# Performance work log

Measured on AMD Instinct MI355X. Metric: run time of the kernel, lower is better.

## Reference

```python
import jax, jax.numpy as jnp
import numpy as np

D_MODEL = 1024
NUM_HEADS = 16
D_K = D_MODEL // NUM_HEADS
ROPE_THETA = 10000.0


def apply_rope(x, pos):
    # x: [B, nh, S, d_k], pos: [S]
    d = x.shape[-1]
    inv_freq = ROPE_THETA ** (-jnp.arange(0, d, 2, dtype=jnp.float32) / d)  # [d/2]
    ang = pos.astype(jnp.float32)[:, None] * inv_freq[None, :]              # [S, d/2]
    cos, sin = jnp.cos(ang), jnp.sin(ang)
    x1, x2 = x[..., 0::2], x[..., 1::2]
    out_even = x1 * cos - x2 * sin
    out_odd = x1 * sin + x2 * cos
    return jnp.stack([out_even, out_odd], axis=-1).reshape(x.shape)


def setup_inputs() -> dict:
    key = jax.random.key(0)
    kx, kq, kk, kv, ko = jax.random.split(key, 5)
    B, S = 4, 2048
    std = np.sqrt(2.0 / (D_MODEL + D_MODEL))
    x = jax.random.normal(kx, (B, S, D_MODEL), dtype=jnp.float32)
    q_proj = jax.random.normal(kq, (D_MODEL, D_MODEL), dtype=jnp.float32) * std
    k_proj = jax.random.normal(kk, (D_MODEL, D_MODEL), dtype=jnp.float32) * std
    v_proj = jax.random.normal(kv, (D_MODEL, D_MODEL), dtype=jnp.float32) * std
    o_proj = jax.random.normal(ko, (D_MODEL, D_MODEL), dtype=jnp.float32) * std
    return {"x": x, "q_proj": q_proj, "k_proj": k_proj, "v_proj": v_proj, "o_proj": o_proj}


def reference(x, q_proj, k_proj, v_proj, o_proj):
    B, S, D = x.shape
    nh, dk = NUM_HEADS, D // NUM_HEADS
    # projections: weights stored [d_out, d_in] -> x @ W.T
    def split_heads(t):
        return t.reshape(B, S, nh, dk).transpose(0, 2, 1, 3)  # [B, nh, S, dk]
    q = split_heads(x @ q_proj.T)
    k = split_heads(x @ k_proj.T)
    v = split_heads(x @ v_proj.T)
    pos = jnp.arange(S)
    q = apply_rope(q, pos)
    k = apply_rope(k, pos)
    scores = jnp.einsum('bhqd,bhkd->bhqk', q, k) / jnp.sqrt(jnp.float32(dk))
    causal = jnp.tril(jnp.ones((S, S), dtype=bool))
    scores = jnp.where(causal, scores, -jnp.inf)
    attn = jax.nn.softmax(scores, axis=-1)
    out = jnp.einsum('bhqk,bhkd->bhqd', attn, v)          # [B, nh, S, dk]
    out = out.transpose(0, 2, 1, 3).reshape(B, S, D)      # merge heads
    return out @ o_proj.T
```

## Files before the change

### kernel.cpp

```cpp
#include <hip/hip_runtime.h>
#include <hip/hip_bf16.h>
#include <cstdint>


typedef __attribute__((ext_vector_type(8))) short short8;
typedef __attribute__((ext_vector_type(4))) float float4v;

#define MFMA16(a, b, c) __builtin_amdgcn_mfma_f32_16x16x32_bf16((a), (b), (c), 0, 0, 0)

__device__ __forceinline__ void glds16(const void* g, void* l) {
    __builtin_amdgcn_global_load_lds(
        (const __attribute__((address_space(1))) void*)g,
        (__attribute__((address_space(3))) void*)l, 16, 0, 0);
}

__device__ __forceinline__ unsigned int pk2(float a, float b) {
    __hip_bfloat162 h = __float22bfloat162_rn(make_float2(a, b));
    union { __hip_bfloat162 h; unsigned int u; } v; v.h = h;
    return v.u;
}

__device__ __forceinline__ unsigned short f2bf(float x) {
    union { float f; unsigned int u; } v; v.f = x;
    unsigned int r = (v.u + 0x7FFFu + ((v.u >> 16) & 1u)) >> 16;
    return (unsigned short)r;
}

__device__ __forceinline__ float bf2f(unsigned short b) {
    union { unsigned int u; float f; } v; v.u = ((unsigned int)b) << 16;
    return v.f;
}

__device__ __forceinline__ short8 load8f(const float* p) {
    const float4 f0 = *(const float4*)p;
    const float4 f1 = *(const float4*)(p + 4);
    union { short8 s; unsigned int u[4]; } r;
    r.u[0] = pk2(f0.x, f0.y);
    r.u[1] = pk2(f0.z, f0.w);
    r.u[2] = pk2(f1.x, f1.y);
    r.u[3] = pk2(f1.z, f1.w);
    return r.s;
}

__global__ __launch_bounds__(256) void convert_kernel(
    const float* __restrict__ in, __hip_bfloat16* __restrict__ out)
{
    const int idx = (blockIdx.x * 256 + threadIdx.x) * 8;
    *(short8*)(out + idx) = load8f(in + idx);
}

__global__ __launch_bounds__(256) void convert4_kernel(
    const float* __restrict__ a, const float* __restrict__ b,
    const float* __restrict__ c, const float* __restrict__ d,
    __hip_bfloat16* __restrict__ oa, __hip_bfloat16* __restrict__ ob,
    __hip_bfloat16* __restrict__ oc, __hip_bfloat16* __restrict__ od)
{
    const int m = blockIdx.x >> 9;
    const float* in = (m == 0) ? a : (m == 1) ? b : (m == 2) ? c : d;
    __hip_bfloat16* out = (m == 0) ? oa : (m == 1) ? ob : (m == 2) ? oc : od;
    const int idx = ((blockIdx.x & 511) * 256 + threadIdx.x) * 8;
    *(short8*)(out + idx) = load8f(in + idx);
}

__global__ __launch_bounds__(256) void rope_table_kernel(float2* __restrict__ table)
{
    const int idx = blockIdx.x * 256 + threadIdx.x;
    const int pos = idx >> 5, fi = idx & 31;
    const float f = exp2f(-(float)fi * (13.287712379549449f / 32.0f));
    float sn, cs;
    sincosf((float)pos * f, &sn, &cs);
    table[idx] = make_float2(cs, sn);
}

__global__ __launch_bounds__(256) void rope2_kernel(
    __hip_bfloat16* __restrict__ Qp, __hip_bfloat16* __restrict__ Kp,
    const float2* __restrict__ table)
{
    const int sel = blockIdx.x >> 14;
    __hip_bfloat16* T = sel ? Kp : Qp;
    const float scale = sel ? 1.0f : 0.18033688011112042f;
    const int idx = (blockIdx.x & 16383) * 256 + threadIdx.x;
    const int r = idx >> 9;
    const int p = idx & 511;
    const int h = p >> 5, i = p & 31;
    const float2 cs = table[(r & 2047) * 32 + i];
    unsigned short* ptr = (unsigned short*)T + (int64_t)r * 1024 + h * 64 + 2 * i;
    const ushort2 xv = *(const ushort2*)ptr;
    const float x1 = bf2f(xv.x), x2 = bf2f(xv.y);
    const unsigned int o = pk2((x1 * cs.x - x2 * cs.y) * scale,
                               (x1 * cs.y + x2 * cs.x) * scale);
    *(unsigned int*)ptr = o;
}

template<int BBF>
__global__ __launch_bounds__(256) void qkv_gemm(
    const __hip_bfloat16* __restrict__ Abf,
    const void* __restrict__ Wq, const void* __restrict__ Wk, const void* __restrict__ Wv,
    __hip_bfloat16* __restrict__ Qp, __hip_bfloat16* __restrict__ Kp,
    __hip_bfloat16* __restrict__ Vt)
{
    __shared__ unsigned short smem[128 * 128];

    const int K = 1024;
    const int bm = blockIdx.x / 24, bn = blockIdx.x % 24;
    const int widx = bn >> 3;
    const int bcol0 = (bn & 7) * 128;
    const void* W = (widx == 0) ? Wq : (widx == 1) ? Wk : Wv;

    const int tid = threadIdx.x;
    const int wave = tid >> 6, lane = tid & 63;
    const int wm = (wave >> 1) * 64, wn = (wave & 1) * 64;
    const int m16 = lane & 15, quad = lane >> 4;

    const int lrow = lane >> 2, lcol = (lane & 3) * 8;
    const int srow = tid >> 2, scol = (tid & 3) * 8;

    float4v acc[4][4] = {};

    for (int k0 = 0; k0 < K; k0 += 32) {
        short8 rb0, rb1;
        if (!BBF) {
            const float* Wf = (const float*)W;
            rb0 = load8f(Wf + (int64_t)(bcol0 + srow) * K + scol + k0);
            rb1 = load8f(Wf + (int64_t)(bcol0 + 64 + srow) * K + scol + k0);
        }
        __syncthreads();
        {
            const __hip_bfloat16* g = Abf + (int64_t)(bm * 128 + wave * 32 + lrow) * K + lcol + k0;
            glds16(g, &smem[wave * 1024]);
            glds16(g + (int64_t)16 * K, &smem[wave * 1024 + 512]);
        }
        if (BBF) {
            const __hip_bfloat16* g = (const __hip_bfloat16*)W +
                (int64_t)(bcol0 + wave * 32 + lrow) * K + lcol + k0;
            glds16(g, &smem[4096 + wave * 1024]);
            glds16(g + (int64_t)16 * K, &smem[4096 + wave * 1024 + 512]);
        } else {
            *(short8*)&smem[4096 + srow * 32 + scol] = rb0;
            *(short8*)&smem[4096 + (64 + srow) * 32 + scol] = rb1;
        }
        __syncthreads();

        short8 af[4], bf[4];
#pragma unroll
        for (int i = 0; i < 4; i++)
            af[i] = *(const short8*)&smem[(wm + i * 16 + m16) * 32 + quad * 8];
#pragma unroll
        for (int j = 0; j < 4; j++)
            bf[j] = *(const short8*)&smem[4096 + (wn + j * 16 + m16) * 32 + quad * 8];
#pragma unroll
        for (int i = 0; i < 4; i++)
#pragma unroll
            for (int j = 0; j < 4; j++)
                acc[i][j] = MFMA16(af[i], bf[j], acc[i][j]);
    }

    if (widx == 2) {
        __syncthreads();
#pragma unroll
        for (int i = 0; i < 4; i++)
#pragma unroll
            for (int j = 0; j < 4; j++) {
                const int col = wn + j * 16 + m16;
                const int key = (col & 7) * 8;
#pragma unroll
                for (int r = 0; r < 4; r++) {
                    const int row = wm + i * 16 + quad * 4 + r;
                    smem[col * 128 + (row ^ key)] = f2bf(acc[i][j][r]);
                }
            }
        __syncthreads();
        const int dc = tid >> 4;
        const int seg = (tid & 15) * 8;
#pragma unroll
        for (int pass = 0; pass < 8; pass++) {
            const int dcol = pass * 16 + dc;
            const short8 v = *(const short8*)&smem[dcol * 128 + (seg ^ ((dcol & 7) * 8))];
            *(short8*)((unsigned short*)Vt + (int64_t)(bcol0 + dcol) * 8192 + bm * 128 + seg) = v;
        }
    } else {
        __hip_bfloat16* dst = (widx == 0) ? Qp : Kp;
        const int row0 = bm * 128 + wm + quad * 4;
        const int col0 = bcol0 + wn + m16;
#pragma unroll
        for (int i = 0; i < 4; i++)
#pragma unroll
            for (int j = 0; j < 4; j++)
#pragma unroll
                for (int r = 0; r < 4; r++)
                    dst[(int64_t)(row0 + i * 16 + r) * 1024 + col0 + j * 16] =
                        __float2bfloat16(acc[i][j][r]);
    }
}

template<int BBF>
__global__ __launch_bounds__(256) void gemm_o(
    const __hip_bfloat16* __restrict__ Abf, const void* __restrict__ B,
    float* __restrict__ C, int M, int N, int K)
{
    __shared__ __hip_bfloat16 lA[128 * 32];
    __shared__ __hip_bfloat16 lB[64 * 32];

    const int nb = N >> 6;
    const int bm = blockIdx.x / nb, bn = blockIdx.x % nb;
    const int tid = threadIdx.x;
    const int wave = tid >> 6, lane = tid & 63;
    const int wm = (wave >> 1) * 64, wn = (wave & 1) * 32;
    const int m16 = lane & 15, quad = lane >> 4;
    const int lrow = lane >> 2, lcol = (lane & 3) * 8;
    const int srow = tid >> 2, scol = (tid & 3) * 8;

    float4v acc[4][2] = {};

    for (int k0 = 0; k0 < K; k0 += 32) {
        short8 rb0;
        if (!BBF) {
            const float* Bf = (const float*)B;
            rb0 = load8f(Bf + (int64_t)(bn * 64 + srow) * K + scol + k0);
        }
        __syncthreads();
        {
            const __hip_bfloat16* g = Abf + (int64_t)(bm * 128 + wave * 32 + lrow) * K + lcol + k0;
            glds16(g, &lA[wave * 1024]);
            glds16(g + (int64_t)16 * K, &lA[wave * 1024 + 512]);
        }
        if (BBF) {
            glds16((const __hip_bfloat16*)B +
                   (int64_t)(bn * 64 + wave * 16 + (lane >> 2)) * K + lcol + k0,
                   &lB[wave * 512]);
        } else {
            *(short8*)&lB[srow * 32 + scol] = rb0;
        }
        __syncthreads();

        short8 af[4], bf[2];
#pragma unroll
        for (int i = 0; i < 4; i++)
            af[i] = *(const short8*)&lA[(wm + i * 16 + m16) * 32 + quad * 8];
#pragma unroll
        for (int j = 0; j < 2; j++)
            bf[j] = *(const short8*)&lB[(wn + j * 16 + m16) * 32 + quad * 8];
#pragma unroll
        for (int i = 0; i < 4; i++)
#pragma unroll
            for (int j = 0; j < 2; j++)
                acc[i][j] = MFMA16(af[i], bf[j], acc[i][j]);
    }

    const int row0 = bm * 128 + wm + quad * 4;
    const int col0 = bn * 64 + wn + m16;
#pragma unroll
    for (int i = 0; i < 4; i++)
#pragma unroll
        for (int j = 0; j < 2; j++)
#pragma unroll
            for (int r = 0; r < 4; r++)
                C[(int64_t)(row0 + i * 16 + r) * N + col0 + j * 16] = acc[i][j][r];
}

__global__ __launch_bounds__(256) void attn_kernel(
    const __hip_bfloat16* __restrict__ Q,
    const __hip_bfloat16* __restrict__ Kg,
    const __hip_bfloat16* __restrict__ Vt,
    __hip_bfloat16* __restrict__ O,
    int S, int BS)
{
    const int g = blockIdx.x >> 6;
    const int qt = (g < 4) ? 15 - g : (g < 8) ? 11 - g : (g < 12) ? g : g - 12;
    const int bh = blockIdx.x & 63;
    const int b = bh >> 4, h = bh & 15;
    const int tid = threadIdx.x;
    const int wave = tid >> 6, lane = tid & 63;
    const int m16 = lane & 15, quad = lane >> 4;

    __shared__ __hip_bfloat16 lK[64 * 64];
    __shared__ __hip_bfloat16 lV[64 * 64];
    __shared__ __hip_bfloat16 lP[4][32 * 64];

    const int qrow0 = qt * 128 + wave * 32;
    const int64_t rowbase = (int64_t)b * S;

    short8 aq[2][2];
#pragma unroll
    for (int i = 0; i < 2; i++) {
        const __hip_bfloat16* qp = Q + (rowbase + qrow0 + i * 16 + m16) * 1024 + h * 64 + quad * 8;
        aq[i][0] = *(const short8*)qp;
        aq[i][1] = *(const short8*)(qp + 32);
    }

    float lsum[2] = {0.f, 0.f};
    float4v o_acc[2][4] = {};

    const int srow = tid >> 3;
    const int scol = (tid & 7) * 8;

    const int ktmax_blk = 2 * qt + 1;
    const int ktmax_w = 2 * qt + (wave >> 1);
    const int k8 = (m16 & 7) * 8;

    short8 pk0, pk1, pv0, pv1;
#define PREFETCH(KT)                                                                          \
    do {                                                                                      \
        pk0 = *(const short8*)(Kg + (rowbase + (KT) * 64 + srow) * 1024 + h * 64 + scol);     \
        pk1 = *(const short8*)(Kg + (rowbase + (KT) * 64 + srow + 32) * 1024 + h * 64 + scol);\
        pv0 = *(const short8*)(Vt + (int64_t)(h * 64 + srow) * BS + rowbase + (KT) * 64 + scol);      \
        pv1 = *(const short8*)(Vt + (int64_t)(h * 64 + srow + 32) * BS + rowbase + (KT) * 64 + scol); \
    } while (0)

    PREFETCH(0);

    for (int kt = 0; kt <= ktmax_blk; kt++) {
        __syncthreads();
        *(short8*)&lK[srow * 64 + (scol ^ ((srow & 7) * 8))] = pk0;
        *(short8*)&lK[(srow + 32) * 64 + (scol ^ (((srow + 32) & 7) * 8))] = pk1;
        *(short8*)&lV[srow * 64 + (scol ^ ((srow & 7) * 8))] = pv0;
        *(short8*)&lV[(srow + 32) * 64 + (scol ^ (((srow + 32) & 7) * 8))] = pv1;
        __syncthreads();

        if (kt < ktmax_blk) PREFETCH(kt + 1);

        if (kt <= ktmax_w) {
            float4v st[4][2] = {};
#pragma unroll
            for (int mi = 0; mi < 4; mi++) {
                const int n = mi * 16 + m16;
                const int sw = (n & 7) * 8;
                short8 k0 = *(const short8*)&lK[n * 64 + ((quad * 8) ^ sw)];
                short8 k1 = *(const short8*)&lK[n * 64 + ((32 + quad * 8) ^ sw)];
#pragma unroll
                for (int ni = 0; ni < 2; ni++) {
                    st[mi][ni] = MFMA16(k0, aq[ni][0], st[mi][ni]);
                    st[mi][ni] = MFMA16(k1, aq[ni][1], st[mi][ni]);
                }
            }

            const bool need_mask = (kt * 64 + 63 > qrow0);
#pragma unroll
            for (int ni = 0; ni < 2; ni++) {
                const int qg = qrow0 + ni * 16 + m16;
#pragma unroll
                for (int mi = 0; mi < 4; mi++) {
                    float p[4];
#pragma unroll
                    for (int r = 0; r < 4; r++) {
                        p[r] = exp2f(st[mi][ni][r]);
                        if (need_mask) {
                            const int kvg = kt * 64 + mi * 16 + quad * 4 + r;
                            if (kvg > qg) p[r] = 0.0f;
                        }
                    }
                    lsum[ni] += (p[0] + p[1]) + (p[2] + p[3]);
                    uint2 w;
                    w.x = pk2(p[0], p[1]);
                    w.y = pk2(p[2], p[3]);
                    *(uint2*)&lP[wave][(ni * 16 + m16) * 64 + ((mi * 16 + quad * 4) ^ k8)] = w;
                }
            }

            short8 ap[2][2];
#pragma unroll
            for (int i = 0; i < 2; i++)
#pragma unroll
                for (int ks = 0; ks < 2; ks++)
                    ap[i][ks] = *(const short8*)
                        &lP[wave][(i * 16 + m16) * 64 + ((ks * 32 + quad * 8) ^ k8)];
#pragma unroll
            for (int jd = 0; jd < 4; jd++) {
                const int d = jd * 16 + m16;
                const int sw = (d & 7) * 8;
                short8 b0 = *(const short8*)&lV[d * 64 + ((quad * 8) ^ sw)];
                short8 b1 = *(const short8*)&lV[d * 64 + ((32 + quad * 8) ^ sw)];
#pragma unroll
                for (int i = 0; i < 2; i++) {
                    o_acc[i][jd] = MFMA16(ap[i][0], b0, o_acc[i][jd]);
                    o_acc[i][jd] = MFMA16(ap[i][1], b1, o_acc[i][jd]);
                }
            }
        }
    }
#undef PREFETCH

    float rinv[2];
#pragma unroll
    for (int ni = 0; ni < 2; ni++) {
        float v = lsum[ni];
        v += __shfl_xor(v, 16);
        v += __shfl_xor(v, 32);
        rinv[ni] = 1.0f / v;
    }
    float ri[2][4];
#pragma unroll
    for (int i = 0; i < 2; i++)
#pragma unroll
        for (int r = 0; r < 4; r++)
            ri[i][r] = __shfl(rinv[i], quad * 4 + r);

#pragma unroll
    for (int i = 0; i < 2; i++)
#pragma unroll
        for (int jd = 0; jd < 4; jd++)
#pragma unroll
            for (int r = 0; r < 4; r++) {
                const int row = qrow0 + i * 16 + quad * 4 + r;
                O[(rowbase + row) * 1024 + h * 64 + jd * 16 + m16] =
                    __float2bfloat16(o_acc[i][jd][r] * ri[i][r]);
            }
}

extern "C" void kernel_launch(void* const* d_in, const int* in_sizes, int n_in,
                              void* d_out, int out_size, void* d_ws, size_t ws_size,
                              hipStream_t stream)
{
    const float* x  = (const float*)d_in[0];
    const float* qw = (const float*)d_in[1];
    const float* kw = (const float*)d_in[2];
    const float* vw = (const float*)d_in[3];
    const float* ow = (const float*)d_in[4];

    const int BS = 8192, D = 1024, S = 2048;
    const size_t MiB = 1024 * 1024;

    char* ws = (char*)d_ws;
    __hip_bfloat16* xb  = (__hip_bfloat16*)(ws);
    __hip_bfloat16* Qb  = (__hip_bfloat16*)(ws + 16 * MiB);
    __hip_bfloat16* Kb  = (__hip_bfloat16*)(ws + 32 * MiB);
    __hip_bfloat16* Vtb = (__hip_bfloat16*)(ws + 48 * MiB);
    __hip_bfloat16* wqb = (__hip_bfloat16*)(ws + 64 * MiB);
    __hip_bfloat16* wkb = (__hip_bfloat16*)(ws + 66 * MiB);
    __hip_bfloat16* wvb = (__hip_bfloat16*)(ws + 68 * MiB);
    __hip_bfloat16* wob = (__hip_bfloat16*)(ws + 70 * MiB);
    float2* table = (float2*)(ws);
    const bool wbf = ws_size >= 72 * MiB;

    dim3 blk(256);
    convert_kernel<<<(BS * D) / 2048, blk, 0, stream>>>(x, xb);
    if (wbf) {
        convert4_kernel<<<4 * (D * D) / 2048, blk, 0, stream>>>(
            qw, kw, vw, ow, wqb, wkb, wvb, wob);
        qkv_gemm<1><<<64 * 24, blk, 0, stream>>>(xb, wqb, wkb, wvb, Qb, Kb, Vtb);
    } else {
        qkv_gemm<0><<<64 * 24, blk, 0, stream>>>(xb, qw, kw, vw, Qb, Kb, Vtb);
    }
    rope_table_kernel<<<256, blk, 0, stream>>>(table);
    rope2_kernel<<<2 * 16384, blk, 0, stream>>>(Qb, Kb, table);
    attn_kernel<<<4 * 16 * (S / 128), blk, 0, stream>>>(Qb, Kb, Vtb, Qb , S, BS);
    if (wbf) gemm_o<1><<<(BS / 128) * (D / 64), blk, 0, stream>>>(Qb, wob, (float*)d_out, BS, D, D);
    else     gemm_o<0><<<(BS / 128) * (D / 64), blk, 0, stream>>>(Qb, ow,  (float*)d_out, BS, D, D);
}
```

Baseline: 287.9 us.

## Double GEMM K-tile to 64 with XOR-swizzled LDS layout in QKV and O projections

Both projection GEMMs now stage 64-wide K slices per iteration instead of 32, which halves the number of barrier pairs and global-load rounds per tile. The LDS layout is XOR-swizzled by row so that 128-byte rows do not cause bank conflicts on MFMA fragment reads. The cost is twice the shared memory per block for the O GEMM and more registers for the staged fp32 weight conversions, which can lower occupancy.

```diff
diff --git a/kernel.cpp b/kernel.cpp
--- a/kernel.cpp
+++ b/kernel.cpp
@@ -112,47 +112,60 @@
     const int wm = (wave >> 1) * 64, wn = (wave & 1) * 64;
     const int m16 = lane & 15, quad = lane >> 4;
 
-    const int lrow = lane >> 2, lcol = (lane & 3) * 8;
+    const int grow = lane >> 3;
+    const int gcolsw = ((lane & 7) ^ (lane >> 3)) * 8;
     const int srow = tid >> 2, scol = (tid & 3) * 8;
 
     float4v acc[4][4] = {};
 
-    for (int k0 = 0; k0 < K; k0 += 32) {
-        short8 rb0, rb1;
+    for (int k0 = 0; k0 < K; k0 += 64) {
+        short8 rb[4];
         if (!BBF) {
             const float* Wf = (const float*)W;
-            rb0 = load8f(Wf + (int64_t)(bcol0 + srow) * K + scol + k0);
-            rb1 = load8f(Wf + (int64_t)(bcol0 + 64 + srow) * K + scol + k0);
+#pragma unroll
+            for (int t = 0; t < 4; t++)
+                rb[t] = load8f(Wf + (int64_t)(bcol0 + (t >> 1) * 64 + srow) * K
+                               + k0 + (t & 1) * 32 + scol);
         }
         __syncthreads();
         {
-            const __hip_bfloat16* g = Abf + (int64_t)(bm * 128 + wave * 32 + lrow) * K + lcol + k0;
-            glds16(g, &smem[wave * 1024]);
-            glds16(g + (int64_t)16 * K, &smem[wave * 1024 + 512]);
+            const __hip_bfloat16* g = Abf + (int64_t)(bm * 128 + wave * 32 + grow) * K + k0 + gcolsw;
+#pragma unroll
+            for (int t = 0; t < 4; t++)
+                glds16(g + (int64_t)(t * 8) * K, &smem[(wave * 32 + t * 8) * 64]);
         }
         if (BBF) {
             const __hip_bfloat16* g = (const __hip_bfloat16*)W +
-                (int64_t)(bcol0 + wave * 32 + lrow) * K + lcol + k0;
-            glds16(g, &smem[4096 + wave * 1024]);
-            glds16(g + (int64_t)16 * K, &smem[4096 + wave * 1024 + 512]);
+                (int64_t)(bcol0 + wave * 32 + grow) * K + k0 + gcolsw;
+#pragma unroll
+            for (int t = 0; t < 4; t++)
+                glds16(g + (int64_t)(t * 8) * K, &smem[8192 + (wave * 32 + t * 8) * 64]);
         } else {
-            *(short8*)&smem[4096 + srow * 32 + scol] = rb0;
-            *(short8*)&smem[4096 + (64 + srow) * 32 + scol] = rb1;
-        }
-        __syncthreads();
-
-        short8 af[4], bf[4];
-#pragma unroll
-        for (int i = 0; i < 4; i++)
-            af[i] = *(const short8*)&smem[(wm + i * 16 + m16) * 32 + quad * 8];
-#pragma unroll
-        for (int j = 0; j < 4; j++)
-            bf[j] = *(const short8*)&smem[4096 + (wn + j * 16 + m16) * 32 + quad * 8];
-#pragma unroll
-        for (int i = 0; i < 4; i++)
+#pragma unroll
+            for (int t = 0; t < 4; t++) {
+                const int r = (t >> 1) * 64 + srow;
+                const int c = (t & 1) * 32 + scol;
+                *(short8*)&smem[8192 + r * 64 + (c ^ ((r & 7) * 8))] = rb[t];
+            }
+        }
+        __syncthreads();
+
+#pragma unroll
+        for (int kk = 0; kk < 2; kk++) {
+            const int ksw = (kk * 32 + quad * 8) ^ ((m16 & 7) * 8);
+            short8 af[4], bf[4];
+#pragma unroll
+            for (int i = 0; i < 4; i++)
+                af[i] = *(const short8*)&smem[(wm + i * 16 + m16) * 64 + ksw];
 #pragma unroll
             for (int j = 0; j < 4; j++)
-                acc[i][j] = MFMA16(af[i], bf[j], acc[i][j]);
+                bf[j] = *(const short8*)&smem[8192 + (wn + j * 16 + m16) * 64 + ksw];
+#pragma unroll
+            for (int i = 0; i < 4; i++)
+#pragma unroll
+                for (int j = 0; j < 4; j++)
+                    acc[i][j] = MFMA16(af[i], bf[j], acc[i][j]);
+        }
     }
 
     if (widx == 2) {
@@ -198,8 +211,8 @@
     const __hip_bfloat16* __restrict__ Abf, const void* __restrict__ B,
     float* __restrict__ C, int M, int N, int K)
 {
-    __shared__ __hip_bfloat16 lA[128 * 32];
-    __shared__ __hip_bfloat16 lB[64 * 32];
+    __shared__ __hip_bfloat16 lA[128 * 64];
+    __shared__ __hip_bfloat16 lB[64 * 64];
 
     const int nb = N >> 6;
     const int bm = blockIdx.x / nb, bn = blockIdx.x % nb;
@@ -207,44 +220,58 @@
     const int wave = tid >> 6, lane = tid & 63;
     const int wm = (wave >> 1) * 64, wn = (wave & 1) * 32;
     const int m16 = lane & 15, quad = lane >> 4;
-    const int lrow = lane >> 2, lcol = (lane & 3) * 8;
-    const int srow = tid >> 2, scol = (tid & 3) * 8;
+    const int grow = lane >> 3;
+    const int gcolsw = ((lane & 7) ^ (lane >> 3)) * 8;
+    const int srow = tid >> 3, scol = (tid & 7) * 8;
 
     float4v acc[4][2] = {};
 
-    for (int k0 = 0; k0 < K; k0 += 32) {
-        short8 rb0;
+    for (int k0 = 0; k0 < K; k0 += 64) {
+        short8 rb[2];
         if (!BBF) {
             const float* Bf = (const float*)B;
-            rb0 = load8f(Bf + (int64_t)(bn * 64 + srow) * K + scol + k0);
+#pragma unroll
+            for (int t = 0; t < 2; t++)
+                rb[t] = load8f(Bf + (int64_t)(bn * 64 + t * 32 + srow) * K + k0 + scol);
         }
         __syncthreads();
         {
-            const __hip_bfloat16* g = Abf + (int64_t)(bm * 128 + wave * 32 + lrow) * K + lcol + k0;
-            glds16(g, &lA[wave * 1024]);
-            glds16(g + (int64_t)16 * K, &lA[wave * 1024 + 512]);
+            const __hip_bfloat16* g = Abf + (int64_t)(bm * 128 + wave * 32 + grow) * K + k0 + gcolsw;
+#pragma unroll
+            for (int t = 0; t < 4; t++)
+                glds16(g + (int64_t)(t * 8) * K, &lA[(wave * 32 + t * 8) * 64]);
         }
         if (BBF) {
-            glds16((const __hip_bfloat16*)B +
-                   (int64_t)(bn * 64 + wave * 16 + (lane >> 2)) * K + lcol + k0,
-                   &lB[wave * 512]);
+            const __hip_bfloat16* g = (const __hip_bfloat16*)B +
+                (int64_t)(bn * 64 + wave * 16 + grow) * K + k0 + gcolsw;
+#pragma unroll
+            for (int t = 0; t < 2; t++)
+                glds16(g + (int64_t)(t * 8) * K, &lB[(wave * 16 + t * 8) * 64]);
         } else {
-            *(short8*)&lB[srow * 32 + scol] = rb0;
-        }
-        __syncthreads();
-
-        short8 af[4], bf[2];
-#pragma unroll
-        for (int i = 0; i < 4; i++)
-            af[i] = *(const short8*)&lA[(wm + i * 16 + m16) * 32 + quad * 8];
-#pragma unroll
-        for (int j = 0; j < 2; j++)
-            bf[j] = *(const short8*)&lB[(wn + j * 16 + m16) * 32 + quad * 8];
-#pragma unroll
-        for (int i = 0; i < 4; i++)
+#pragma unroll
+            for (int t = 0; t < 2; t++) {
+                const int r = t * 32 + srow;
+                *(short8*)&lB[r * 64 + (scol ^ ((r & 7) * 8))] = rb[t];
+            }
+        }
+        __syncthreads();
+
+#pragma unroll
+        for (int kk = 0; kk < 2; kk++) {
+            const int ksw = (kk * 32 + quad * 8) ^ ((m16 & 7) * 8);
+            short8 af[4], bf[2];
+#pragma unroll
+            for (int i = 0; i < 4; i++)
+                af[i] = *(const short8*)&lA[(wm + i * 16 + m16) * 64 + ksw];
 #pragma unroll
             for (int j = 0; j < 2; j++)
-                acc[i][j] = MFMA16(af[i], bf[j], acc[i][j]);
+                bf[j] = *(const short8*)&lB[(wn + j * 16 + m16) * 64 + ksw];
+#pragma unroll
+            for (int i = 0; i < 4; i++)
+#pragma unroll
+                for (int j = 0; j < 2; j++)
+                    acc[i][j] = MFMA16(af[i], bf[j], acc[i][j]);
+        }
     }
 
     const int row0 = bm * 128 + wm + quad * 4;
```

Measured after the change: 265.4 us. 7.8% less time.
